# Kernel optimization log

Measured on AMD Instinct MI355X. Metric: run time of the kernel, lower is better.

## Reference

```python
import jax, jax.numpy as jnp
import numpy as np

EMBED = 512
HEADS = 1
HEAD_DIM = EMBED // HEADS  # 512 (heads must be 1 for the original torch code to run)
N, S = 4, 4096


def setup_inputs() -> dict:
    key = jax.random.key(0)
    ks = jax.random.split(key, 9)
    scale = 1.0 / np.sqrt(EMBED)
    return {
        "values": jax.random.normal(ks[0], (N, 1, S, EMBED), dtype=jnp.float32),
        "keys": jax.random.normal(ks[1], (N, 1, S, EMBED), dtype=jnp.float32),
        "query": jax.random.normal(ks[2], (N, 1, S, EMBED), dtype=jnp.float32),
        "mask": jax.random.randint(ks[3], (N, 1, S, S), 0, 2, dtype=jnp.int32),
        "Wv": jax.random.normal(ks[4], (EMBED, EMBED), dtype=jnp.float32) * scale,
        "Wk": jax.random.normal(ks[5], (EMBED, EMBED), dtype=jnp.float32) * scale,
        "Wq": jax.random.normal(ks[6], (EMBED, EMBED), dtype=jnp.float32) * scale,
        "Wo": jax.random.normal(ks[7], (EMBED, EMBED), dtype=jnp.float32) * scale,
        "bo": jnp.zeros((EMBED,), dtype=jnp.float32),
    }


def reference(values, keys, query, mask, Wv, Wk, Wq, Wo, bo):
    n = query.shape[0]
    q_len = query.shape[2]
    # reshape(N, -1, heads, head_dim); inputs are [N, 1, S, E] -> [N, S, H, Dh]
    v = values.reshape(n, -1, HEADS, HEAD_DIM)
    k = keys.reshape(n, -1, HEADS, HEAD_DIM)
    q = query.reshape(n, -1, HEADS, HEAD_DIM)
    # per-module linear projections (nn.Linear: y = x @ W.T)
    v = jnp.einsum('nlhd,ed->nlhe', v, Wv)
    k = jnp.einsum('nlhd,ed->nlhe', k, Wk)
    q = jnp.einsum('nqhd,ed->nqhe', q, Wq)
    # full [N, H, Q, K] score matrix, as in the original
    energy = jnp.einsum('nqhd,nkhd->nhqk', q, k)
    energy = jnp.where(mask == 0, jnp.float32(-1e20), energy)
    attn = jax.nn.softmax(energy / np.sqrt(HEAD_DIM), axis=3)
    out = jnp.einsum('nhql,nlhd->nqhd', attn, v).reshape(n, q_len, HEADS * HEAD_DIM)
    return out @ Wo.T + bo
```

## Files before the change

### kernel.cpp

```cpp
#include <hip/hip_runtime.h>

typedef __bf16 bf16x8 __attribute__((ext_vector_type(8)));
typedef float f32x4 __attribute__((ext_vector_type(4)));

#define MFMA(a, b, c) __builtin_amdgcn_mfma_f32_16x16x32_bf16((a), (b), (c), 0, 0, 0)

static constexpr int SEQ = 4096;
static constexpr int DIM = 512;

__device__ __forceinline__ bf16x8 cvt8(const float* __restrict__ p) {
    float4 f0 = *(const float4*)p;
    float4 f1 = *(const float4*)(p + 4);
    bf16x8 v;
    v[0] = (__bf16)f0.x; v[1] = (__bf16)f0.y; v[2] = (__bf16)f0.z; v[3] = (__bf16)f0.w;
    v[4] = (__bf16)f1.x; v[5] = (__bf16)f1.y; v[6] = (__bf16)f1.z; v[7] = (__bf16)f1.w;
    return v;
}

template <bool QKV, bool A_F32, bool OUT_BF16, bool BIAS>
__global__ __launch_bounds__(256, 2)
void gemm128(const void* __restrict__ A0, const void* __restrict__ A1,
             const void* __restrict__ A2, const float* __restrict__ B0,
             const float* __restrict__ B1, const float* __restrict__ B2,
             void* __restrict__ C0, void* __restrict__ C1, void* __restrict__ C2,
             const float* __restrict__ bias, int M, int N, int K)
{
    const void* Ap = A0;
    const float* Bp = B0;
    void* Cp = C0;
    if (QKV) {
        const int z = blockIdx.z;
        Ap = (z == 0) ? A0 : (z == 1) ? A1 : A2;
        Bp = (z == 0) ? B0 : (z == 1) ? B1 : B2;
        Cp = (z == 0) ? C0 : (z == 1) ? C1 : C2;
    }
    __shared__ __bf16 As[128 * 64];
    __shared__ __bf16 Bs[128 * 64];
    const int tid  = threadIdx.x;
    const int wave = tid >> 6;
    const int lane = tid & 63;
    const int quad = lane >> 4;
    const int l16  = lane & 15;
    const int m0 = blockIdx.x * 128;
    const int n0 = blockIdx.y * 128;
    const int wm = (wave >> 1) * 64;
    const int wn = (wave & 1) * 64;
    const int srow = tid >> 3;
    const int slc  = tid & 7;

    f32x4 acc[4][4] = {};

    for (int k0 = 0; k0 < K; k0 += 64) {
        #pragma unroll
        for (int i = 0; i < 4; i++) {
            const int row = srow + 32 * i;
            const int pc  = slc ^ (row & 7);
            bf16x8 va, vb;
            if (A_F32) va = cvt8((const float*)Ap + (size_t)(m0 + row) * K + k0 + slc * 8);
            else       va = *(const bf16x8*)((const __bf16*)Ap + (size_t)(m0 + row) * K + k0 + slc * 8);
            vb = cvt8(Bp + (size_t)(n0 + row) * K + k0 + slc * 8);
            *(bf16x8*)&As[row * 64 + pc * 8] = va;
            *(bf16x8*)&Bs[row * 64 + pc * 8] = vb;
        }
        __syncthreads();
        #pragma unroll
        for (int kk = 0; kk < 2; kk++) {
            bf16x8 af[4], bg[4];
            #pragma unroll
            for (int mt = 0; mt < 4; mt++) {
                const int r = wm + mt * 16 + l16;
                af[mt] = *(const bf16x8*)&As[r * 64 + ((kk * 4 + quad) ^ (r & 7)) * 8];
            }
            #pragma unroll
            for (int nt = 0; nt < 4; nt++) {
                const int r = wn + nt * 16 + l16;
                bg[nt] = *(const bf16x8*)&Bs[r * 64 + ((kk * 4 + quad) ^ (r & 7)) * 8];
            }
            #pragma unroll
            for (int mt = 0; mt < 4; mt++)
                #pragma unroll
                for (int nt = 0; nt < 4; nt++)
                    acc[mt][nt] = MFMA(af[mt], bg[nt], acc[mt][nt]);
        }
        __syncthreads();
    }
    #pragma unroll
    for (int mt = 0; mt < 4; mt++)
        #pragma unroll
        for (int nt = 0; nt < 4; nt++)
            #pragma unroll
            for (int r = 0; r < 4; r++) {
                const int row = m0 + wm + mt * 16 + quad * 4 + r;
                const int col = n0 + wn + nt * 16 + l16;
                float v = acc[mt][nt][r];
                if (BIAS) v += bias[col];
                if (OUT_BF16) ((__bf16*)Cp)[(size_t)row * N + col] = (__bf16)v;
                else          ((float*)Cp)[(size_t)row * N + col] = v;
            }
}

__global__ __launch_bounds__(256)
void transpose_bf16(const __bf16* __restrict__ in, __bf16* __restrict__ out)
{
    __shared__ __bf16 T[64][72];
    const int nb = blockIdx.z;
    const int s0 = blockIdx.x * 64;
    const int d0 = blockIdx.y * 64;
    const int t = threadIdx.x;
    const int r = t >> 3;
    const int c = (t & 7) * 8;
    const __bf16* src = in + (size_t)nb * SEQ * DIM;
    __bf16* dst = out + (size_t)nb * DIM * SEQ;
    #pragma unroll
    for (int rr = 0; rr < 64; rr += 32) {
        bf16x8 v = *(const bf16x8*)(src + (size_t)(s0 + r + rr) * DIM + d0 + c);
        *(bf16x8*)&T[r + rr][c] = v;
    }
    __syncthreads();
    #pragma unroll
    for (int rr = 0; rr < 64; rr += 32) {
        bf16x8 v;
        #pragma unroll
        for (int i = 0; i < 8; i++) v[i] = T[c + i][r + rr];
        *(bf16x8*)(dst + (size_t)(d0 + r + rr) * SEQ + s0 + c) = v;
    }
}

__global__ __launch_bounds__(512, 2)
void flash_attn(const __bf16* __restrict__ Qp, const __bf16* __restrict__ Kp,
                const __bf16* __restrict__ Vt, const int* __restrict__ mask,
                __bf16* __restrict__ AO)
{
    constexpr float SCALE = 0.044194173824159216f;

    __shared__ __bf16 Qs[64 * 512];
    __shared__ __bf16 P[64 * 256];
    __shared__ unsigned Wb[64 * 8];
    __shared__ float pmax[8][72];
    __shared__ float psum[8][72];
    __shared__ float m_s[2][64];
    __shared__ float alpha_s[64];
    __shared__ float l_s[64];
    __shared__ unsigned flag_s;

    const int n  = blockIdx.y;
    const int q0 = blockIdx.x * 64;
    const int tid  = threadIdx.x;
    const int nw   = tid >> 6;
    const int lane = tid & 63;
    const int quad = lane >> 4;
    const int l16  = lane & 15;

    const __bf16* Qb = Qp + (size_t)n * SEQ * DIM;
    const __bf16* Kb = Kp + (size_t)n * SEQ * DIM;
    const __bf16* Vb = Vt + (size_t)n * DIM * SEQ;
    const int*    Mb = mask + (size_t)n * SEQ * SEQ;

    #pragma unroll
    for (int i = 0; i < 8; i++) {
        const int idx = i * 512 + tid;
        const int row = idx >> 6;
        const int lc  = idx & 63;
        const int pc  = (lc & 56) | ((lc & 7) ^ (row & 7));
        *(bf16x8*)&Qs[row * 512 + pc * 8] =
            *(const bf16x8*)(Qb + (size_t)(q0 + row) * DIM + lc * 8);
    }
    if (tid < 64) { m_s[0][tid] = -__builtin_inff(); l_s[tid] = 0.f; }
    __syncthreads();

    f32x4 o[4][4] = {};

    for (int j = 0; j < 16; j++) {
        const int k0 = j * 256;
        const int jp = j & 1;

        {
            const int* mp = Mb + (size_t)(q0 + (tid >> 3)) * SEQ + k0 + (tid & 7) * 32;
            unsigned w = 0;
            #pragma unroll
            for (int c = 0; c < 8; c++) {
                int4 m4 = *(const int4*)(mp + c * 4);
                w |= (unsigned)(m4.x & 1) << (c * 4 + 0);
                w |= (unsigned)(m4.y & 1) << (c * 4 + 1);
                w |= (unsigned)(m4.z & 1) << (c * 4 + 2);
                w |= (unsigned)(m4.w & 1) << (c * 4 + 3);
            }
            Wb[tid] = w;
        }

        f32x4 s[4][2] = {};
        {
            const __bf16* kb = Kb + (size_t)(k0 + nw * 32 + l16) * DIM + quad * 8;
            #pragma unroll
            for (int kk = 0; kk < 16; kk++) {
                bf16x8 b0 = *(const bf16x8*)(kb + kk * 32);
                bf16x8 b1 = *(const bf16x8*)(kb + 16 * DIM + kk * 32);
                const int lc = kk * 4 + quad;
                #pragma unroll
                for (int g = 0; g < 4; g++) {
                    const int row = g * 16 + l16;
                    bf16x8 a = *(const bf16x8*)&Qs[row * 512 + ((lc & 56) | ((lc & 7) ^ (row & 7))) * 8];
                    s[g][0] = MFMA(a, b0, s[g][0]);
                    s[g][1] = MFMA(a, b1, s[g][1]);
                }
            }
        }
        #pragma unroll
        for (int g = 0; g < 4; g++) {
            f32x4 v;
            #pragma unroll
            for (int r = 0; r < 4; r++) v[r] = fmaxf(s[g][0][r], s[g][1][r]);
            #pragma unroll
            for (int d = 1; d < 16; d <<= 1) {
                #pragma unroll
                for (int r = 0; r < 4; r++) v[r] = fmaxf(v[r], __shfl_xor(v[r], d));
            }
            if (l16 == 0) {
                #pragma unroll
                for (int r = 0; r < 4; r++) pmax[nw][g * 16 + quad * 4 + r] = v[r];
            }
        }
        __syncthreads();

        if (nw == 0) {
            float mp_ = pmax[0][lane];
            #pragma unroll
            for (int w2 = 1; w2 < 8; w2++) mp_ = fmaxf(mp_, pmax[w2][lane]);
            mp_ *= SCALE;
            const float mo = m_s[jp][lane];
            const float mn = fmaxf(mo, mp_);
            m_s[jp ^ 1][lane] = mn;
            alpha_s[lane] = __expf(mo - mn);
            unsigned long long ch = __ballot(mn > mo);
            if (lane == 0) flag_s = (unsigned)(ch | (ch >> 32));
        }
        __syncthreads();

        if (flag_s) {
            #pragma unroll
            for (int g = 0; g < 4; g++) {
                const float4 al = *(const float4*)&alpha_s[g * 16 + quad * 4];
                #pragma unroll
                for (int dt = 0; dt < 4; dt++)
                    #pragma unroll
                    for (int r = 0; r < 4; r++)
                        o[g][dt][r] *= ((const float*)&al)[r];
            }
        }
        const float* mnew = m_s[jp ^ 1];
        #pragma unroll
        for (int g = 0; g < 4; g++) {
            const float4 mn4 = *(const float4*)&mnew[g * 16 + quad * 4];
            f32x4 prow = {};
            #pragma unroll
            for (int r = 0; r < 4; r++) {
                const int row = g * 16 + quad * 4 + r;
                const unsigned wq = Wb[row * 8 + nw];
                #pragma unroll
                for (int nt = 0; nt < 2; nt++) {
                    float p = __expf(s[g][nt][r] * SCALE - ((const float*)&mn4)[r]);
                    p = ((wq >> (nt * 16 + l16)) & 1u) ? p : 0.f;
                    prow[r] += p;
                    const int col = nw * 32 + nt * 16 + l16;
                    const int ch2 = col >> 3;
                    const int pc  = (ch2 & 24) | ((ch2 & 7) ^ (row & 7));
                    P[row * 256 + pc * 8 + (col & 7)] = (__bf16)p;
                }
            }
            #pragma unroll
            for (int d = 1; d < 16; d <<= 1) {
                #pragma unroll
                for (int r = 0; r < 4; r++) prow[r] += __shfl_xor(prow[r], d);
            }
            if (l16 == 0) {
                #pragma unroll
                for (int r = 0; r < 4; r++) psum[nw][g * 16 + quad * 4 + r] = prow[r];
            }
        }
        __syncthreads();

        if (nw == 0) {
            float acc = psum[0][lane];
            #pragma unroll
            for (int w2 = 1; w2 < 8; w2++) acc += psum[w2][lane];
            l_s[lane] = l_s[lane] * alpha_s[lane] + acc;
        }
        {
            const __bf16* vb = Vb + (size_t)(nw * 64 + l16) * SEQ + k0 + quad * 8;
            #pragma unroll
            for (int kk = 0; kk < 8; kk++) {
                bf16x8 pa[4];
                const int lc = kk * 4 + quad;
                #pragma unroll
                for (int g = 0; g < 4; g++) {
                    const int row = g * 16 + l16;
                    pa[g] = *(const bf16x8*)&P[row * 256 + ((lc & 24) | ((lc & 7) ^ (row & 7))) * 8];
                }
                #pragma unroll
                for (int dt = 0; dt < 4; dt++) {
                    bf16x8 b = *(const bf16x8*)(vb + (size_t)(dt * 16) * SEQ + kk * 32);
                    #pragma unroll
                    for (int g = 0; g < 4; g++)
                        o[g][dt] = MFMA(pa[g], b, o[g][dt]);
                }
            }
        }
    }

    __syncthreads();
    #pragma unroll
    for (int g = 0; g < 4; g++) {
        const float4 l4 = *(const float4*)&l_s[g * 16 + quad * 4];
        float li[4];
        #pragma unroll
        for (int r = 0; r < 4; r++) li[r] = 1.f / ((const float*)&l4)[r];
        #pragma unroll
        for (int dt = 0; dt < 4; dt++)
            #pragma unroll
            for (int r = 0; r < 4; r++)
                AO[(size_t)(n * SEQ + q0 + g * 16 + quad * 4 + r) * DIM + nw * 64 + dt * 16 + l16]
                    = (__bf16)(o[g][dt][r] * li[r]);
    }
}

extern "C" void kernel_launch(void* const* d_in, const int* in_sizes, int n_in,
                              void* d_out, int out_size, void* d_ws, size_t ws_size,
                              hipStream_t stream)
{
    const float* values = (const float*)d_in[0];
    const float* keys   = (const float*)d_in[1];
    const float* query  = (const float*)d_in[2];
    const int*   mask   = (const int*)d_in[3];
    const float* Wv = (const float*)d_in[4];
    const float* Wk = (const float*)d_in[5];
    const float* Wq = (const float*)d_in[6];
    const float* Wo = (const float*)d_in[7];
    const float* bo = (const float*)d_in[8];
    float* out = (float*)d_out;

    char* ws = (char*)d_ws;
    __bf16* Qp = (__bf16*)(ws);
    __bf16* Kp = (__bf16*)(ws + (16u << 20));
    __bf16* Vp = (__bf16*)(ws + (32u << 20));
    __bf16* Vt = (__bf16*)(ws + (48u << 20));
    __bf16* AO = Vp;

    const int M = 4 * SEQ;

    dim3 gproj(M / 128, DIM / 128, 3);
    gemm128<true, true, true, false><<<gproj, 256, 0, stream>>>(
        query, keys, values, Wq, Wk, Wv, Qp, Kp, Vp, nullptr, M, DIM, DIM);

    dim3 gtr(SEQ / 64, DIM / 64, 4);
    transpose_bf16<<<gtr, 256, 0, stream>>>(Vp, Vt);

    dim3 gfa(SEQ / 64, 4);
    flash_attn<<<gfa, 512, 0, stream>>>(Qp, Kp, Vt, mask, AO);

    dim3 gout(M / 128, DIM / 128, 1);
    gemm128<false, false, false, true><<<gout, 256, 0, stream>>>(
        AO, nullptr, nullptr, Wo, nullptr, nullptr, out, nullptr, nullptr, bo, M, DIM, DIM);
}
```

Before: 836.3 us.

## Rework pipeline: bf16 weight pre-convert, async LDS loads, fused V transpose, 32x32 MFMA attention

Weights are converted to bf16 once in a small kernel, and the projection and output GEMMs load tiles with global_load_lds straight into LDS without swizzling. The V transpose moves into the QKV GEMM epilogue, which removes a kernel and a round trip of V through memory. Flash attention now runs 1024-thread blocks over 512-wide key tiles using 32x32x16 MFMAs and writes its output in place over Q. In exchange, the unswizzled LDS reads may cause bank conflicts, and the larger blocks lower occupancy.

```diff
diff --git a/kernel.cpp b/kernel.cpp
--- a/kernel.cpp
+++ b/kernel.cpp
@@ -2,13 +2,22 @@
 
 typedef __bf16 bf16x8 __attribute__((ext_vector_type(8)));
 typedef float f32x4 __attribute__((ext_vector_type(4)));
-
-#define MFMA(a, b, c) __builtin_amdgcn_mfma_f32_16x16x32_bf16((a), (b), (c), 0, 0, 0)
+typedef float f32x16 __attribute__((ext_vector_type(16)));
+
+#define MFMA16(a, b, c) __builtin_amdgcn_mfma_f32_16x16x32_bf16((a), (b), (c), 0, 0, 0)
+#define MFMA32(a, b, c) __builtin_amdgcn_mfma_f32_32x32x16_bf16((a), (b), (c), 0, 0, 0)
 
 static constexpr int SEQ = 4096;
 static constexpr int DIM = 512;
 
-__device__ __forceinline__ bf16x8 cvt8(const float* __restrict__ p) {
+typedef __attribute__((address_space(3))) void lds_void;
+typedef __attribute__((address_space(1))) const void gbl_void;
+
+__device__ __forceinline__ void glds16(const void* g, void* l) {
+    __builtin_amdgcn_global_load_lds((gbl_void*)g, (lds_void*)l, 16, 0, 0);
+}
+
+__device__ __forceinline__ bf16x8 cvt8f(const float* __restrict__ p) {
     float4 f0 = *(const float4*)p;
     float4 f1 = *(const float4*)(p + 4);
     bf16x8 v;
@@ -17,25 +26,32 @@
     return v;
 }
 
-template <bool QKV, bool A_F32, bool OUT_BF16, bool BIAS>
-__global__ __launch_bounds__(256, 2)
-void gemm128(const void* __restrict__ A0, const void* __restrict__ A1,
-             const void* __restrict__ A2, const float* __restrict__ B0,
-             const float* __restrict__ B1, const float* __restrict__ B2,
-             void* __restrict__ C0, void* __restrict__ C1, void* __restrict__ C2,
-             const float* __restrict__ bias, int M, int N, int K)
+__global__ __launch_bounds__(256)
+void convert_w(const float* __restrict__ wq, const float* __restrict__ wk,
+               const float* __restrict__ wv, const float* __restrict__ wo,
+               __bf16* __restrict__ out)
 {
-    const void* Ap = A0;
-    const float* Bp = B0;
-    void* Cp = C0;
-    if (QKV) {
-        const int z = blockIdx.z;
-        Ap = (z == 0) ? A0 : (z == 1) ? A1 : A2;
-        Bp = (z == 0) ? B0 : (z == 1) ? B1 : B2;
-        Cp = (z == 0) ? C0 : (z == 1) ? C1 : C2;
-    }
-    __shared__ __bf16 As[128 * 64];
-    __shared__ __bf16 Bs[128 * 64];
+    const int z = blockIdx.y;
+    const float* src = (z == 0) ? wq : (z == 1) ? wk : (z == 2) ? wv : wo;
+    __bf16* dst = out + (size_t)z * DIM * DIM;
+    const int i = (blockIdx.x * 256 + threadIdx.x) * 8;
+    *(bf16x8*)(dst + i) = cvt8f(src + i);
+}
+
+__global__ __launch_bounds__(256, 3)
+void gemm_qkv(const float* __restrict__ q, const float* __restrict__ k,
+              const float* __restrict__ v, const __bf16* __restrict__ wbf,
+              __bf16* __restrict__ Qp, __bf16* __restrict__ Kp,
+              __bf16* __restrict__ Vt)
+{
+    __shared__ __align__(16) char smem[49152];
+    float* Af  = (float*)smem;
+    __bf16* Bs = (__bf16*)(smem + 32768);
+
+    const int z = blockIdx.z;
+    const float* Ap = (z == 0) ? q : (z == 1) ? k : v;
+    const __bf16* Bp = wbf + (size_t)z * DIM * DIM;
+
     const int tid  = threadIdx.x;
     const int wave = tid >> 6;
     const int lane = tid & 63;
@@ -45,22 +61,23 @@
     const int n0 = blockIdx.y * 128;
     const int wm = (wave >> 1) * 64;
     const int wn = (wave & 1) * 64;
-    const int srow = tid >> 3;
-    const int slc  = tid & 7;
 
     f32x4 acc[4][4] = {};
 
-    for (int k0 = 0; k0 < K; k0 += 64) {
+    for (int k0 = 0; k0 < DIM; k0 += 64) {
+        #pragma unroll
+        for (int i = 0; i < 8; i++) {
+            const int j = wave * 8 + i;
+            const int c = j * 64 + lane;
+            const int row = c >> 4, f4 = c & 15;
+            glds16(Ap + (size_t)(m0 + row) * DIM + k0 + f4 * 4, &Af[j * 256]);
+        }
         #pragma unroll
         for (int i = 0; i < 4; i++) {
-            const int row = srow + 32 * i;
-            const int pc  = slc ^ (row & 7);
-            bf16x8 va, vb;
-            if (A_F32) va = cvt8((const float*)Ap + (size_t)(m0 + row) * K + k0 + slc * 8);
-            else       va = *(const bf16x8*)((const __bf16*)Ap + (size_t)(m0 + row) * K + k0 + slc * 8);
-            vb = cvt8(Bp + (size_t)(n0 + row) * K + k0 + slc * 8);
-            *(bf16x8*)&As[row * 64 + pc * 8] = va;
-            *(bf16x8*)&Bs[row * 64 + pc * 8] = vb;
+            const int j = wave * 4 + i;
+            const int c = j * 64 + lane;
+            const int row = c >> 3, c8 = c & 7;
+            glds16(Bp + (size_t)(n0 + row) * DIM + k0 + c8 * 8, &Bs[j * 512]);
         }
         __syncthreads();
         #pragma unroll
@@ -69,18 +86,100 @@
             #pragma unroll
             for (int mt = 0; mt < 4; mt++) {
                 const int r = wm + mt * 16 + l16;
-                af[mt] = *(const bf16x8*)&As[r * 64 + ((kk * 4 + quad) ^ (r & 7)) * 8];
+                af[mt] = cvt8f(&Af[r * 64 + kk * 32 + quad * 8]);
             }
             #pragma unroll
             for (int nt = 0; nt < 4; nt++) {
                 const int r = wn + nt * 16 + l16;
-                bg[nt] = *(const bf16x8*)&Bs[r * 64 + ((kk * 4 + quad) ^ (r & 7)) * 8];
+                bg[nt] = *(const bf16x8*)&Bs[r * 64 + kk * 32 + quad * 8];
             }
             #pragma unroll
             for (int mt = 0; mt < 4; mt++)
                 #pragma unroll
                 for (int nt = 0; nt < 4; nt++)
-                    acc[mt][nt] = MFMA(af[mt], bg[nt], acc[mt][nt]);
+                    acc[mt][nt] = MFMA16(af[mt], bg[nt], acc[mt][nt]);
+        }
+        __syncthreads();
+    }
+
+    if (z < 2) {
+        __bf16* Cp = (z == 0) ? Qp : Kp;
+        #pragma unroll
+        for (int mt = 0; mt < 4; mt++)
+            #pragma unroll
+            for (int nt = 0; nt < 4; nt++)
+                #pragma unroll
+                for (int r = 0; r < 4; r++)
+                    Cp[(size_t)(m0 + wm + mt * 16 + quad * 4 + r) * DIM
+                       + n0 + wn + nt * 16 + l16] = (__bf16)acc[mt][nt][r];
+    } else {
+        __bf16* Tt = (__bf16*)smem;
+        #pragma unroll
+        for (int mt = 0; mt < 4; mt++)
+            #pragma unroll
+            for (int nt = 0; nt < 4; nt++)
+                #pragma unroll
+                for (int r = 0; r < 4; r++)
+                    Tt[(wm + mt * 16 + quad * 4 + r) * 130 + wn + nt * 16 + l16]
+                        = (__bf16)acc[mt][nt][r];
+        __syncthreads();
+        const int nb = m0 >> 12;
+        const int s0 = m0 & 4095;
+        const int d  = tid >> 1;
+        const int sh = (tid & 1) * 64;
+        __bf16* dst = Vt + (size_t)nb * DIM * SEQ + (size_t)(n0 + d) * SEQ + s0 + sh;
+        #pragma unroll
+        for (int i = 0; i < 8; i++) {
+            bf16x8 vv;
+            #pragma unroll
+            for (int e = 0; e < 8; e++) vv[e] = Tt[(sh + i * 8 + e) * 130 + d];
+            *(bf16x8*)(dst + i * 8) = vv;
+        }
+    }
+}
+
+__global__ __launch_bounds__(256, 3)
+void gemm_out(const __bf16* __restrict__ Ap, const __bf16* __restrict__ Bp,
+              float* __restrict__ Cp, const float* __restrict__ bias)
+{
+    __shared__ __align__(16) __bf16 As[128 * 64];
+    __shared__ __align__(16) __bf16 Bs[128 * 64];
+    const int tid  = threadIdx.x;
+    const int wave = tid >> 6;
+    const int lane = tid & 63;
+    const int quad = lane >> 4;
+    const int l16  = lane & 15;
+    const int m0 = blockIdx.x * 128;
+    const int n0 = blockIdx.y * 128;
+    const int wm = (wave >> 1) * 64;
+    const int wn = (wave & 1) * 64;
+
+    f32x4 acc[4][4] = {};
+
+    for (int k0 = 0; k0 < DIM; k0 += 64) {
+        #pragma unroll
+        for (int i = 0; i < 4; i++) {
+            const int j = wave * 4 + i;
+            const int c = j * 64 + lane;
+            const int row = c >> 3, c8 = c & 7;
+            glds16(Ap + (size_t)(m0 + row) * DIM + k0 + c8 * 8, &As[j * 512]);
+            glds16(Bp + (size_t)(n0 + row) * DIM + k0 + c8 * 8, &Bs[j * 512]);
+        }
+        __syncthreads();
+        #pragma unroll
+        for (int kk = 0; kk < 2; kk++) {
+            bf16x8 af[4], bg[4];
+            #pragma unroll
+            for (int mt = 0; mt < 4; mt++)
+                af[mt] = *(const bf16x8*)&As[(wm + mt * 16 + l16) * 64 + kk * 32 + quad * 8];
+            #pragma unroll
+            for (int nt = 0; nt < 4; nt++)
+                bg[nt] = *(const bf16x8*)&Bs[(wn + nt * 16 + l16) * 64 + kk * 32 + quad * 8];
+            #pragma unroll
+            for (int mt = 0; mt < 4; mt++)
+                #pragma unroll
+                for (int nt = 0; nt < 4; nt++)
+                    acc[mt][nt] = MFMA16(af[mt], bg[nt], acc[mt][nt]);
         }
         __syncthreads();
     }
@@ -90,92 +189,64 @@
         for (int nt = 0; nt < 4; nt++)
             #pragma unroll
             for (int r = 0; r < 4; r++) {
-                const int row = m0 + wm + mt * 16 + quad * 4 + r;
                 const int col = n0 + wn + nt * 16 + l16;
-                float v = acc[mt][nt][r];
-                if (BIAS) v += bias[col];
-                if (OUT_BF16) ((__bf16*)Cp)[(size_t)row * N + col] = (__bf16)v;
-                else          ((float*)Cp)[(size_t)row * N + col] = v;
-            }
-}
-
-__global__ __launch_bounds__(256)
-void transpose_bf16(const __bf16* __restrict__ in, __bf16* __restrict__ out)
-{
-    __shared__ __bf16 T[64][72];
-    const int nb = blockIdx.z;
-    const int s0 = blockIdx.x * 64;
-    const int d0 = blockIdx.y * 64;
-    const int t = threadIdx.x;
-    const int r = t >> 3;
-    const int c = (t & 7) * 8;
-    const __bf16* src = in + (size_t)nb * SEQ * DIM;
-    __bf16* dst = out + (size_t)nb * DIM * SEQ;
-    #pragma unroll
-    for (int rr = 0; rr < 64; rr += 32) {
-        bf16x8 v = *(const bf16x8*)(src + (size_t)(s0 + r + rr) * DIM + d0 + c);
-        *(bf16x8*)&T[r + rr][c] = v;
-    }
-    __syncthreads();
-    #pragma unroll
-    for (int rr = 0; rr < 64; rr += 32) {
-        bf16x8 v;
-        #pragma unroll
-        for (int i = 0; i < 8; i++) v[i] = T[c + i][r + rr];
-        *(bf16x8*)(dst + (size_t)(d0 + r + rr) * SEQ + s0 + c) = v;
-    }
-}
-
-__global__ __launch_bounds__(512, 2)
-void flash_attn(const __bf16* __restrict__ Qp, const __bf16* __restrict__ Kp,
-                const __bf16* __restrict__ Vt, const int* __restrict__ mask,
-                __bf16* __restrict__ AO)
+                Cp[(size_t)(m0 + wm + mt * 16 + quad * 4 + r) * DIM + col]
+                    = acc[mt][nt][r] + bias[col];
+            }
+}
+
+__global__ __launch_bounds__(1024)
+void flash_attn(__bf16* __restrict__ Qp, const __bf16* __restrict__ Kp,
+                const __bf16* __restrict__ Vt, const int* __restrict__ mask)
 {
     constexpr float SCALE = 0.044194173824159216f;
 
     __shared__ __bf16 Qs[64 * 512];
-    __shared__ __bf16 P[64 * 256];
-    __shared__ unsigned Wb[64 * 8];
-    __shared__ float pmax[8][72];
-    __shared__ float psum[8][72];
+    __shared__ __bf16 P[64 * 512];
+    __shared__ unsigned Wb2[16 * 64];
+    __shared__ float pmax[16][68];
+    __shared__ float psum[16][68];
     __shared__ float m_s[2][64];
     __shared__ float alpha_s[64];
     __shared__ float l_s[64];
     __shared__ unsigned flag_s;
 
-    const int n  = blockIdx.y;
-    const int q0 = blockIdx.x * 64;
+    const int bid = blockIdx.x;
+    const int n  = bid & 3;
+    const int q0 = (bid >> 2) * 64;
     const int tid  = threadIdx.x;
     const int nw   = tid >> 6;
     const int lane = tid & 63;
-    const int quad = lane >> 4;
-    const int l16  = lane & 15;
+    const int l32  = lane & 31;
+    const int half = lane >> 5;
 
     const __bf16* Qb = Qp + (size_t)n * SEQ * DIM;
     const __bf16* Kb = Kp + (size_t)n * SEQ * DIM;
     const __bf16* Vb = Vt + (size_t)n * DIM * SEQ;
     const int*    Mb = mask + (size_t)n * SEQ * SEQ;
+    __bf16*       AO = Qp + (size_t)n * SEQ * DIM;
 
     #pragma unroll
-    for (int i = 0; i < 8; i++) {
-        const int idx = i * 512 + tid;
+    for (int i = 0; i < 4; i++) {
+        const int idx = i * 1024 + tid;
         const int row = idx >> 6;
-        const int lc  = idx & 63;
-        const int pc  = (lc & 56) | ((lc & 7) ^ (row & 7));
+        const int c   = idx & 63;
+        const int pc  = (c & 56) | ((c & 7) ^ (row & 7));
         *(bf16x8*)&Qs[row * 512 + pc * 8] =
-            *(const bf16x8*)(Qb + (size_t)(q0 + row) * DIM + lc * 8);
+            *(const bf16x8*)(Qb + (size_t)(q0 + row) * DIM + c * 8);
     }
     if (tid < 64) { m_s[0][tid] = -__builtin_inff(); l_s[tid] = 0.f; }
     __syncthreads();
 
-    f32x4 o[4][4] = {};
-
-    for (int j = 0; j < 16; j++) {
-        const int k0 = j * 256;
+    f32x16 o0 = {}, o1 = {};
+
+    for (int j = 0; j < 8; j++) {
+        const int k0 = j * 512;
         const int jp = j & 1;
 
         {
-            const int* mp = Mb + (size_t)(q0 + (tid >> 3)) * SEQ + k0 + (tid & 7) * 32;
+            const int mr = tid >> 4, wd = tid & 15;
+            const int* mp = Mb + (size_t)(q0 + mr) * SEQ + k0 + wd * 32;
             unsigned w = 0;
             #pragma unroll
             for (int c = 0; c < 8; c++) {
@@ -185,39 +256,37 @@
                 w |= (unsigned)(m4.z & 1) << (c * 4 + 2);
                 w |= (unsigned)(m4.w & 1) << (c * 4 + 3);
             }
-            Wb[tid] = w;
-        }
-
-        f32x4 s[4][2] = {};
+            Wb2[wd * 64 + mr] = w;
+        }
+
+        f32x16 s0 = {}, s1 = {};
         {
-            const __bf16* kb = Kb + (size_t)(k0 + nw * 32 + l16) * DIM + quad * 8;
-            #pragma unroll
-            for (int kk = 0; kk < 16; kk++) {
-                bf16x8 b0 = *(const bf16x8*)(kb + kk * 32);
-                bf16x8 b1 = *(const bf16x8*)(kb + 16 * DIM + kk * 32);
-                const int lc = kk * 4 + quad;
-                #pragma unroll
-                for (int g = 0; g < 4; g++) {
-                    const int row = g * 16 + l16;
-                    bf16x8 a = *(const bf16x8*)&Qs[row * 512 + ((lc & 56) | ((lc & 7) ^ (row & 7))) * 8];
-                    s[g][0] = MFMA(a, b0, s[g][0]);
-                    s[g][1] = MFMA(a, b1, s[g][1]);
+            const __bf16* kb = Kb + (size_t)(k0 + nw * 32 + l32) * DIM + half * 8;
+            #pragma unroll
+            for (int ks = 0; ks < 32; ks++) {
+                bf16x8 b = *(const bf16x8*)(kb + ks * 16);
+                const int c = ks * 2 + half;
+                const int r0 = l32, r1 = 32 + l32;
+                bf16x8 a0 = *(const bf16x8*)&Qs[r0 * 512 + (((c & 56) | ((c & 7) ^ (r0 & 7)))) * 8];
+                bf16x8 a1 = *(const bf16x8*)&Qs[r1 * 512 + (((c & 56) | ((c & 7) ^ (r1 & 7)))) * 8];
+                s0 = MFMA32(a0, b, s0);
+                s1 = MFMA32(a1, b, s1);
+            }
+        }
+        #pragma unroll
+        for (int rt = 0; rt < 2; rt++) {
+            #pragma unroll
+            for (int g2 = 0; g2 < 4; g2++) {
+                f32x4 v;
+                #pragma unroll
+                for (int r = 0; r < 4; r++) v[r] = rt ? s1[g2 * 4 + r] : s0[g2 * 4 + r];
+                #pragma unroll
+                for (int d = 1; d < 32; d <<= 1) {
+                    #pragma unroll
+                    for (int r = 0; r < 4; r++) v[r] = fmaxf(v[r], __shfl_xor(v[r], d));
                 }
-            }
-        }
-        #pragma unroll
-        for (int g = 0; g < 4; g++) {
-            f32x4 v;
-            #pragma unroll
-            for (int r = 0; r < 4; r++) v[r] = fmaxf(s[g][0][r], s[g][1][r]);
-            #pragma unroll
-            for (int d = 1; d < 16; d <<= 1) {
-                #pragma unroll
-                for (int r = 0; r < 4; r++) v[r] = fmaxf(v[r], __shfl_xor(v[r], d));
-            }
-            if (l16 == 0) {
-                #pragma unroll
-                for (int r = 0; r < 4; r++) pmax[nw][g * 16 + quad * 4 + r] = v[r];
+                if (l32 == 0)
+                    *(f32x4*)&pmax[nw][rt * 32 + g2 * 8 + half * 4] = v;
             }
         }
         __syncthreads();
@@ -225,56 +294,57 @@
         if (nw == 0) {
             float mp_ = pmax[0][lane];
             #pragma unroll
-            for (int w2 = 1; w2 < 8; w2++) mp_ = fmaxf(mp_, pmax[w2][lane]);
+            for (int w2 = 1; w2 < 16; w2++) mp_ = fmaxf(mp_, pmax[w2][lane]);
             mp_ *= SCALE;
             const float mo = m_s[jp][lane];
             const float mn = fmaxf(mo, mp_);
             m_s[jp ^ 1][lane] = mn;
             alpha_s[lane] = __expf(mo - mn);
             unsigned long long ch = __ballot(mn > mo);
-            if (lane == 0) flag_s = (unsigned)(ch | (ch >> 32));
+            if (lane == 0) flag_s = (ch != 0ull);
         }
         __syncthreads();
 
         if (flag_s) {
             #pragma unroll
-            for (int g = 0; g < 4; g++) {
-                const float4 al = *(const float4*)&alpha_s[g * 16 + quad * 4];
-                #pragma unroll
-                for (int dt = 0; dt < 4; dt++)
+            for (int rt = 0; rt < 2; rt++)
+                #pragma unroll
+                for (int g2 = 0; g2 < 4; g2++) {
+                    const f32x4 a4 = *(const f32x4*)&alpha_s[rt * 32 + g2 * 8 + half * 4];
                     #pragma unroll
-                    for (int r = 0; r < 4; r++)
-                        o[g][dt][r] *= ((const float*)&al)[r];
-            }
-        }
-        const float* mnew = m_s[jp ^ 1];
-        #pragma unroll
-        for (int g = 0; g < 4; g++) {
-            const float4 mn4 = *(const float4*)&mnew[g * 16 + quad * 4];
-            f32x4 prow = {};
-            #pragma unroll
-            for (int r = 0; r < 4; r++) {
-                const int row = g * 16 + quad * 4 + r;
-                const unsigned wq = Wb[row * 8 + nw];
-                #pragma unroll
-                for (int nt = 0; nt < 2; nt++) {
-                    float p = __expf(s[g][nt][r] * SCALE - ((const float*)&mn4)[r]);
-                    p = ((wq >> (nt * 16 + l16)) & 1u) ? p : 0.f;
-                    prow[r] += p;
-                    const int col = nw * 32 + nt * 16 + l16;
-                    const int ch2 = col >> 3;
-                    const int pc  = (ch2 & 24) | ((ch2 & 7) ^ (row & 7));
-                    P[row * 256 + pc * 8 + (col & 7)] = (__bf16)p;
+                    for (int r = 0; r < 4; r++) {
+                        if (rt) o1[g2 * 4 + r] *= a4[r];
+                        else    o0[g2 * 4 + r] *= a4[r];
+                    }
                 }
-            }
-            #pragma unroll
-            for (int d = 1; d < 16; d <<= 1) {
-                #pragma unroll
-                for (int r = 0; r < 4; r++) prow[r] += __shfl_xor(prow[r], d);
-            }
-            if (l16 == 0) {
-                #pragma unroll
-                for (int r = 0; r < 4; r++) psum[nw][g * 16 + quad * 4 + r] = prow[r];
+        }
+        #pragma unroll
+        for (int rt = 0; rt < 2; rt++) {
+            #pragma unroll
+            for (int g2 = 0; g2 < 4; g2++) {
+                const int rowb = rt * 32 + g2 * 8 + half * 4;
+                const f32x4 m4 = *(const f32x4*)&m_s[jp ^ 1][rowb];
+                const uint4 w4 = *(const uint4*)&Wb2[nw * 64 + rowb];
+                f32x4 ps;
+                #pragma unroll
+                for (int r = 0; r < 4; r++) {
+                    const float sv = rt ? s1[g2 * 4 + r] : s0[g2 * 4 + r];
+                    float p = __expf(sv * SCALE - m4[r]);
+                    const unsigned wb = (&w4.x)[r];
+                    p = ((wb >> l32) & 1u) ? p : 0.f;
+                    ps[r] = p;
+                    const int row = rowb + r;
+                    const int col = nw * 32 + l32;
+                    const int c = col >> 3;
+                    const int pc = (c & 56) | ((c & 7) ^ (row & 7));
+                    P[row * 512 + pc * 8 + (col & 7)] = (__bf16)p;
+                }
+                #pragma unroll
+                for (int d = 1; d < 32; d <<= 1) {
+                    #pragma unroll
+                    for (int r = 0; r < 4; r++) ps[r] += __shfl_xor(ps[r], d);
+                }
+                if (l32 == 0) *(f32x4*)&psum[nw][rowb] = ps;
             }
         }
         __syncthreads();
@@ -282,44 +352,37 @@
         if (nw == 0) {
             float acc = psum[0][lane];
             #pragma unroll
-            for (int w2 = 1; w2 < 8; w2++) acc += psum[w2][lane];
+            for (int w2 = 1; w2 < 16; w2++) acc += psum[w2][lane];
             l_s[lane] = l_s[lane] * alpha_s[lane] + acc;
         }
         {
-            const __bf16* vb = Vb + (size_t)(nw * 64 + l16) * SEQ + k0 + quad * 8;
-            #pragma unroll
-            for (int kk = 0; kk < 8; kk++) {
-                bf16x8 pa[4];
-                const int lc = kk * 4 + quad;
-                #pragma unroll
-                for (int g = 0; g < 4; g++) {
-                    const int row = g * 16 + l16;
-                    pa[g] = *(const bf16x8*)&P[row * 256 + ((lc & 24) | ((lc & 7) ^ (row & 7))) * 8];
-                }
-                #pragma unroll
-                for (int dt = 0; dt < 4; dt++) {
-                    bf16x8 b = *(const bf16x8*)(vb + (size_t)(dt * 16) * SEQ + kk * 32);
-                    #pragma unroll
-                    for (int g = 0; g < 4; g++)
-                        o[g][dt] = MFMA(pa[g], b, o[g][dt]);
-                }
-            }
-        }
-    }
-
+            const __bf16* vb = Vb + (size_t)(nw * 32 + l32) * SEQ + k0 + half * 8;
+            #pragma unroll
+            for (int ks = 0; ks < 32; ks++) {
+                bf16x8 b = *(const bf16x8*)(vb + ks * 16);
+                const int c = ks * 2 + half;
+                const int r0 = l32, r1 = 32 + l32;
+                bf16x8 p0 = *(const bf16x8*)&P[r0 * 512 + (((c & 56) | ((c & 7) ^ (r0 & 7)))) * 8];
+                bf16x8 p1 = *(const bf16x8*)&P[r1 * 512 + (((c & 56) | ((c & 7) ^ (r1 & 7)))) * 8];
+                o0 = MFMA32(p0, b, o0);
+                o1 = MFMA32(p1, b, o1);
+            }
+        }
+    }
     __syncthreads();
+
     #pragma unroll
-    for (int g = 0; g < 4; g++) {
-        const float4 l4 = *(const float4*)&l_s[g * 16 + quad * 4];
-        float li[4];
-        #pragma unroll
-        for (int r = 0; r < 4; r++) li[r] = 1.f / ((const float*)&l4)[r];
-        #pragma unroll
-        for (int dt = 0; dt < 4; dt++)
-            #pragma unroll
-            for (int r = 0; r < 4; r++)
-                AO[(size_t)(n * SEQ + q0 + g * 16 + quad * 4 + r) * DIM + nw * 64 + dt * 16 + l16]
-                    = (__bf16)(o[g][dt][r] * li[r]);
+    for (int rt = 0; rt < 2; rt++) {
+        #pragma unroll
+        for (int g2 = 0; g2 < 4; g2++) {
+            const int rowb = rt * 32 + g2 * 8 + half * 4;
+            const f32x4 l4 = *(const f32x4*)&l_s[rowb];
+            #pragma unroll
+            for (int r = 0; r < 4; r++) {
+                const float ov = rt ? o1[g2 * 4 + r] : o0[g2 * 4 + r];
+                AO[(size_t)(q0 + rowb + r) * DIM + nw * 32 + l32] = (__bf16)(ov / l4[r]);
+            }
+        }
     }
 }
 
@@ -339,25 +402,20 @@
     float* out = (float*)d_out;
 
     char* ws = (char*)d_ws;
-    __bf16* Qp = (__bf16*)(ws);
-    __bf16* Kp = (__bf16*)(ws + (16u << 20));
-    __bf16* Vp = (__bf16*)(ws + (32u << 20));
-    __bf16* Vt = (__bf16*)(ws + (48u << 20));
-    __bf16* AO = Vp;
+    __bf16* Qp  = (__bf16*)(ws);
+    __bf16* Kp  = (__bf16*)(ws + (16u << 20));
+    __bf16* Vt  = (__bf16*)(ws + (32u << 20));
+    __bf16* wbf = (__bf16*)(ws + (48u << 20));
 
     const int M = 4 * SEQ;
 
-    dim3 gproj(M / 128, DIM / 128, 3);
-    gemm128<true, true, true, false><<<gproj, 256, 0, stream>>>(
-        query, keys, values, Wq, Wk, Wv, Qp, Kp, Vp, nullptr, M, DIM, DIM);
-
-    dim3 gtr(SEQ / 64, DIM / 64, 4);
-    transpose_bf16<<<gtr, 256, 0, stream>>>(Vp, Vt);
-
-    dim3 gfa(SEQ / 64, 4);
-    flash_attn<<<gfa, 512, 0, stream>>>(Qp, Kp, Vt, mask, AO);
-
-    dim3 gout(M / 128, DIM / 128, 1);
-    gemm128<false, false, false, true><<<gout, 256, 0, stream>>>(
-        AO, nullptr, nullptr, Wo, nullptr, nullptr, out, nullptr, nullptr, bo, M, DIM, DIM);
-}
+    convert_w<<<dim3(128, 4), 256, 0, stream>>>(Wq, Wk, Wv, Wo, wbf);
+
+    gemm_qkv<<<dim3(M / 128, DIM / 128, 3), 256, 0, stream>>>(
+        query, keys, values, wbf, Qp, Kp, Vt);
+
+    flash_attn<<<256, 1024, 0, stream>>>(Qp, Kp, Vt, mask);
+
+    gemm_out<<<dim3(M / 128, DIM / 128), 256, 0, stream>>>(
+        Qp , wbf + (size_t)3 * DIM * DIM, out, bo);
+}
```

Measured after the change: 1.007 ms. 1.2x slower.
